# Kernel optimization log

Hardware: AMD Instinct MI355X
Metric: run time of the kernel (lower is better)

## Reference

```python
import jax, jax.numpy as jnp
import numpy as np

ALPHA = 0.2          # LeakyReLU negative slope
NEG_INF = -9e15      # mask value used by the torch module


def setup_inputs() -> dict:
    key = jax.random.key(0)
    k1, k2, k3, k4 = jax.random.split(key, 4)
    N, F_IN, F_OUT = 8192, 128, 128
    h = jax.random.normal(k1, (N, F_IN), dtype=jnp.float32)
    adj = jax.random.randint(k2, (N, N), 0, 2, dtype=jnp.int32)
    # xavier_uniform(gain=1.414) approximated with scaled normal init
    W = jax.random.normal(k3, (F_IN, F_OUT), dtype=jnp.float32) * (1.414 / np.sqrt(F_IN))
    a = jax.random.normal(k4, (2 * F_OUT, 1), dtype=jnp.float32) * (1.414 / np.sqrt(2 * F_OUT))
    return {"h": h, "adj": adj, "W": W, "a": a}


def reference(h, adj, W, a):
    # Wh: [N, F]
    Wh = h @ W
    F_out = W.shape[1]
    # e[i,j] = LeakyReLU( [Wh_i || Wh_j] . a ) = LeakyReLU( Wh_i.a1 + Wh_j.a2 )
    e_src = Wh @ a[:F_out, 0]   # [N]
    e_dst = Wh @ a[F_out:, 0]   # [N]
    e = jax.nn.leaky_relu(e_src[:, None] + e_dst[None, :], negative_slope=ALPHA)  # [N, N]
    attention = jax.nn.softmax(jnp.where(adj > 0, e, NEG_INF), axis=1)
    # dropout is identity in eval mode
    h_prime = attention @ Wh    # [N, F]
    return h_prime
```

## Files before the change

kernel.cpp:

```cpp
#include <hip/hip_runtime.h>
#include <hip/hip_bf16.h>


#define NN 8192
#define FF 128
#define SEG 4
#define JSEG (NN / SEG)
#define ITERS (JSEG / 64)

typedef __bf16 bf16x8 __attribute__((ext_vector_type(8)));
typedef float floatx4 __attribute__((ext_vector_type(4)));

__device__ __forceinline__ unsigned short f2b(float f) {
    unsigned int u = __float_as_uint(f);
    return (unsigned short)((u + 0x7FFFu + ((u >> 16) & 1u)) >> 16);
}

__global__ __launch_bounds__(128) void k0_uv(const float* __restrict__ W,
                                             const float* __restrict__ a,
                                             float* __restrict__ u,
                                             float* __restrict__ v) {
    int k = blockIdx.x, t = threadIdx.x;
    float wv = W[k * FF + t];
    float p1 = wv * a[t];
    float p2 = wv * a[FF + t];
    for (int off = 32; off; off >>= 1) {
        p1 += __shfl_down(p1, off);
        p2 += __shfl_down(p2, off);
    }
    __shared__ float r[4];
    if ((t & 63) == 0) { r[(t >> 6) * 2] = p1; r[(t >> 6) * 2 + 1] = p2; }
    __syncthreads();
    if (t == 0) { u[k] = r[0] + r[2]; v[k] = r[1] + r[3]; }
}

__global__ __launch_bounds__(256) void k1_wh(const float* __restrict__ h,
                                             const float* __restrict__ W,
                                             const float* __restrict__ u,
                                             const float* __restrict__ v,
                                             unsigned short* __restrict__ WhT,
                                             float* __restrict__ e_src,
                                             float* __restrict__ e_dst) {
    __shared__ float hL[32 * 132];
    __shared__ float wL[128 * 132];
    __shared__ float uL[128], vL[128];
    __shared__ unsigned short tL[128 * 40];

    int t = threadIdx.x;
    int i0 = blockIdx.x * 32;

    {
        int row = t >> 3, c = (t & 7) * 16;
        const float4* s = (const float4*)&h[(i0 + row) * FF + c];
        float4* d = (float4*)&hL[row * 132 + c];
        #pragma unroll
        for (int j = 0; j < 4; j++) d[j] = s[j];
    }
    {
        int row = t >> 1, c = (t & 1) * 64;
        const float4* s = (const float4*)&W[row * FF + c];
        float4* d = (float4*)&wL[row * 132 + c];
        #pragma unroll
        for (int j = 0; j < 16; j++) d[j] = s[j];
    }
    if (t < 128) { uL[t] = u[t]; vL[t] = v[t]; }
    __syncthreads();

    int r0 = (t & 7) * 4;
    int c0 = (t >> 3) * 4;
    float acc[4][4] = {};
    for (int k0 = 0; k0 < 128; k0 += 4) {
        float4 hr[4], wr[4];
        #pragma unroll
        for (int i = 0; i < 4; i++) hr[i] = *(const float4*)&hL[(r0 + i) * 132 + k0];
        #pragma unroll
        for (int i = 0; i < 4; i++) wr[i] = *(const float4*)&wL[(k0 + i) * 132 + c0];
        #pragma unroll
        for (int kj = 0; kj < 4; kj++) {
            #pragma unroll
            for (int ri = 0; ri < 4; ri++) {
                float hvv = ((const float*)&hr[ri])[kj];
                const float* wvv = (const float*)&wr[kj];
                #pragma unroll
                for (int cj = 0; cj < 4; cj++) acc[ri][cj] = fmaf(hvv, wvv[cj], acc[ri][cj]);
            }
        }
    }
    #pragma unroll
    for (int ri = 0; ri < 4; ri++)
        #pragma unroll
        for (int cj = 0; cj < 4; cj++)
            tL[(c0 + cj) * 40 + r0 + ri] = f2b(acc[ri][cj]);
    __syncthreads();

    if (t < 64) {
        int row = t & 31;
        const float* sv = (t < 32) ? uL : vL;
        float s = 0.f;
        for (int k = 0; k < 128; k += 4) {
            float4 h4 = *(const float4*)&hL[row * 132 + k];
            float4 s4 = *(const float4*)&sv[k];
            s = fmaf(h4.x, s4.x, s); s = fmaf(h4.y, s4.y, s);
            s = fmaf(h4.z, s4.z, s); s = fmaf(h4.w, s4.w, s);
        }
        (t < 32 ? e_src : e_dst)[i0 + row] = s;
    }
    {
        int f = t & 127, half = t >> 7;
        const uint4* s = (const uint4*)&tL[f * 40 + half * 16];
        uint4* d = (uint4*)&WhT[f * NN + i0 + half * 16];
        d[0] = s[0]; d[1] = s[1];
    }
}

__device__ __forceinline__ float mask_w(int a, float x) {
    float l = fmaxf(x, 0.2f * x);
    return a > 0 ? __expf(l) : 0.f;
}

__global__ __launch_bounds__(512, 4) void k2_gat(const int* __restrict__ adj,
                                                 const unsigned short* __restrict__ WhT,
                                                 const float* __restrict__ e_src,
                                                 const float* __restrict__ e_dst,
                                                 float* __restrict__ num,
                                                 float* __restrict__ den) {
    __shared__ unsigned short wt[2][32 * 64];
    __shared__ float esL[32];
    __shared__ float dpart[32 * 17];

    int t = threadIdx.x;
    int bx = blockIdx.x;
    int g = bx >> 2, seg = bx & 3;
    int i0 = g * 32;
    int jbase = seg * JSEG;

    if (t < 32) esL[t] = e_src[i0 + t];

    int ii = t & 31;
    int q  = t >> 5;
    int lane = t & 63, wave = t >> 6;
    int mrow = lane & 15, quad = lane >> 4;
    int n0 = wave * 16;

    const unsigned short* Bb = WhT + (size_t)(n0 + mrow) * NN + jbase + quad * 8;
    const int*   Ab = adj + (size_t)(i0 + ii) * NN + jbase + q * 4;
    const float* Eb = e_dst + jbase + q * 4;

    int waddr = ii * 64 + (((q >> 1) ^ (ii & 7)) << 3) + ((q & 1) << 2);
    int ra00 = mrow * 64 + ((quad ^ (mrow & 7)) << 3);
    int ra01 = mrow * 64 + (((4 + quad) ^ (mrow & 7)) << 3);
    int ra10 = (16 + mrow) * 64 + ((quad ^ (mrow & 7)) << 3);
    int ra11 = (16 + mrow) * 64 + (((4 + quad) ^ (mrow & 7)) << 3);

    floatx4 acc0 = {0.f, 0.f, 0.f, 0.f};
    floatx4 acc1 = {0.f, 0.f, 0.f, 0.f};
    float dsum = 0.f;
    __syncthreads();
    float es_i = esL[ii];

    int4   av = *(const int4*)Ab;
    float4 ed = *(const float4*)Eb;
    bf16x8 b0 = *(const bf16x8*)Bb;
    bf16x8 b1 = *(const bf16x8*)(Bb + 32);
    {
        float w0 = mask_w(av.x, es_i + ed.x);
        float w1 = mask_w(av.y, es_i + ed.y);
        float w2 = mask_w(av.z, es_i + ed.z);
        float w3 = mask_w(av.w, es_i + ed.w);
        dsum += (w0 + w1) + (w2 + w3);
        *(ushort4*)&wt[0][waddr] = make_ushort4(f2b(w0), f2b(w1), f2b(w2), f2b(w3));
    }
    __syncthreads();

    for (int k = 0; k < ITERS - 1; k++) {
        int joff = (k + 1) * 64;
        int4   av2 = *(const int4*)(Ab + joff);
        float4 ed2 = *(const float4*)(Eb + joff);
        bf16x8 nb0 = *(const bf16x8*)(Bb + joff);
        bf16x8 nb1 = *(const bf16x8*)(Bb + joff + 32);

        const unsigned short* buf = wt[k & 1];
        bf16x8 a00 = *(const bf16x8*)&buf[ra00];
        bf16x8 a10 = *(const bf16x8*)&buf[ra10];
        bf16x8 a01 = *(const bf16x8*)&buf[ra01];
        bf16x8 a11 = *(const bf16x8*)&buf[ra11];
        acc0 = __builtin_amdgcn_mfma_f32_16x16x32_bf16(a00, b0, acc0, 0, 0, 0);
        acc1 = __builtin_amdgcn_mfma_f32_16x16x32_bf16(a10, b0, acc1, 0, 0, 0);
        acc0 = __builtin_amdgcn_mfma_f32_16x16x32_bf16(a01, b1, acc0, 0, 0, 0);
        acc1 = __builtin_amdgcn_mfma_f32_16x16x32_bf16(a11, b1, acc1, 0, 0, 0);

        float w0 = mask_w(av2.x, es_i + ed2.x);
        float w1 = mask_w(av2.y, es_i + ed2.y);
        float w2 = mask_w(av2.z, es_i + ed2.z);
        float w3 = mask_w(av2.w, es_i + ed2.w);
        dsum += (w0 + w1) + (w2 + w3);
        *(ushort4*)&wt[(k + 1) & 1][waddr] = make_ushort4(f2b(w0), f2b(w1), f2b(w2), f2b(w3));
        b0 = nb0; b1 = nb1;
        __syncthreads();
    }
    {
        const unsigned short* buf = wt[(ITERS - 1) & 1];
        bf16x8 a00 = *(const bf16x8*)&buf[ra00];
        bf16x8 a10 = *(const bf16x8*)&buf[ra10];
        bf16x8 a01 = *(const bf16x8*)&buf[ra01];
        bf16x8 a11 = *(const bf16x8*)&buf[ra11];
        acc0 = __builtin_amdgcn_mfma_f32_16x16x32_bf16(a00, b0, acc0, 0, 0, 0);
        acc1 = __builtin_amdgcn_mfma_f32_16x16x32_bf16(a10, b0, acc1, 0, 0, 0);
        acc0 = __builtin_amdgcn_mfma_f32_16x16x32_bf16(a01, b1, acc0, 0, 0, 0);
        acc1 = __builtin_amdgcn_mfma_f32_16x16x32_bf16(a11, b1, acc1, 0, 0, 0);
    }

    dpart[ii * 17 + q] = dsum;
    __syncthreads();
    if (t < 32) {
        float s = 0.f;
        #pragma unroll
        for (int k = 0; k < 16; k++) s += dpart[t * 17 + k];
        atomicAdd(&den[i0 + t], s);
    }

    #pragma unroll
    for (int r = 0; r < 4; r++) {
        int row0 = quad * 4 + r;
        atomicAdd(&num[(size_t)(i0 + row0) * FF + n0 + mrow], acc0[r]);
        atomicAdd(&num[(size_t)(i0 + 16 + row0) * FF + n0 + mrow], acc1[r]);
    }
}

__global__ __launch_bounds__(256) void k3_scale(float* __restrict__ out,
                                                const float* __restrict__ den) {
    int idx = blockIdx.x * 256 + threadIdx.x;
    int i = idx >> 5;
    int c = (idx & 31) << 2;
    float r = 1.0f / den[i];
    float4* p = (float4*)&out[(size_t)i * FF + c];
    float4 v = *p;
    v.x *= r; v.y *= r; v.z *= r; v.w *= r;
    *p = v;
}

extern "C" void kernel_launch(void* const* d_in, const int* in_sizes, int n_in,
                              void* d_out, int out_size, void* d_ws, size_t ws_size,
                              hipStream_t stream) {
    const float* h   = (const float*)d_in[0];
    const int*   adj = (const int*)d_in[1];
    const float* W   = (const float*)d_in[2];
    const float* a   = (const float*)d_in[3];
    float* out = (float*)d_out;

    char* ws = (char*)d_ws;
    unsigned short* WhT = (unsigned short*)ws;
    float* u     = (float*)(ws + 2097152);
    float* v     = u + 128;
    float* e_src = v + 128;
    float* e_dst = e_src + NN;
    float* den   = e_dst + NN;

    hipMemsetAsync(out, 0, (size_t)NN * FF * sizeof(float), stream);
    hipMemsetAsync(den, 0, (size_t)NN * sizeof(float), stream);

    k0_uv<<<dim3(128), dim3(128), 0, stream>>>(W, a, u, v);
    k1_wh<<<dim3(256), dim3(256), 0, stream>>>(h, W, u, v, WhT, e_src, e_dst);
    k2_gat<<<dim3(256 * SEG), dim3(512), 0, stream>>>(adj, WhT, e_src, e_dst, out, den);
    k3_scale<<<dim3(NN * FF / 4 / 256), dim3(256), 0, stream>>>(out, den);
}
```

Before: 421.8 us.

## Replace atomic accumulation with per-segment partials and deepen adj prefetch

The attention kernel now writes per-segment numerator and denominator partials with nontemporal stores instead of float atomics. A merge kernel sums the four segments and normalises. This also removes the two memsets. The adjacency and e_dst loads are prefetched two iterations ahead, and the thread-to-row mapping is changed so each row's 64 columns come from 16 consecutive threads, giving more contiguous global reads. The cost is an extra 16 MB of partial writes and reads in the merge step.

```diff
diff --git a/kernel.cpp b/kernel.cpp
--- a/kernel.cpp
+++ b/kernel.cpp
@@ -122,8 +122,8 @@
                                                  const unsigned short* __restrict__ WhT,
                                                  const float* __restrict__ e_src,
                                                  const float* __restrict__ e_dst,
-                                                 float* __restrict__ num,
-                                                 float* __restrict__ den) {
+                                                 float* __restrict__ numpart,
+                                                 float* __restrict__ denpart) {
     __shared__ unsigned short wt[2][32 * 64];
     __shared__ float esL[32];
     __shared__ float dpart[32 * 17];
@@ -136,8 +136,8 @@
 
     if (t < 32) esL[t] = e_src[i0 + t];
 
-    int ii = t & 31;
-    int q  = t >> 5;
+    int q  = t & 15;
+    int ii = t >> 4;
     int lane = t & 63, wave = t >> 6;
     int mrow = lane & 15, quad = lane >> 4;
     int n0 = wave * 16;
@@ -155,29 +155,34 @@
     floatx4 acc0 = {0.f, 0.f, 0.f, 0.f};
     floatx4 acc1 = {0.f, 0.f, 0.f, 0.f};
     float dsum = 0.f;
-    __syncthreads();
-    float es_i = esL[ii];
-
-    int4   av = *(const int4*)Ab;
-    float4 ed = *(const float4*)Eb;
+
+    int4   av0 = *(const int4*)Ab;
+    float4 ed0 = *(const float4*)Eb;
+    int4   avB = *(const int4*)(Ab + 64);
+    float4 edB = *(const float4*)(Eb + 64);
     bf16x8 b0 = *(const bf16x8*)Bb;
     bf16x8 b1 = *(const bf16x8*)(Bb + 32);
-    {
-        float w0 = mask_w(av.x, es_i + ed.x);
-        float w1 = mask_w(av.y, es_i + ed.y);
-        float w2 = mask_w(av.z, es_i + ed.z);
-        float w3 = mask_w(av.w, es_i + ed.w);
+
+    __syncthreads();
+    float es_i = esL[ii];
+
+    {
+        float w0 = mask_w(av0.x, es_i + ed0.x);
+        float w1 = mask_w(av0.y, es_i + ed0.y);
+        float w2 = mask_w(av0.z, es_i + ed0.z);
+        float w3 = mask_w(av0.w, es_i + ed0.w);
         dsum += (w0 + w1) + (w2 + w3);
         *(ushort4*)&wt[0][waddr] = make_ushort4(f2b(w0), f2b(w1), f2b(w2), f2b(w3));
     }
     __syncthreads();
 
     for (int k = 0; k < ITERS - 1; k++) {
-        int joff = (k + 1) * 64;
-        int4   av2 = *(const int4*)(Ab + joff);
-        float4 ed2 = *(const float4*)(Eb + joff);
-        bf16x8 nb0 = *(const bf16x8*)(Bb + joff);
-        bf16x8 nb1 = *(const bf16x8*)(Bb + joff + 32);
+        int jp = ((k + 2 < ITERS) ? (k + 2) : (ITERS - 1)) * 64;
+        int4   avN = *(const int4*)(Ab + jp);
+        float4 edN = *(const float4*)(Eb + jp);
+        int jn = (k + 1) * 64;
+        bf16x8 nb0 = *(const bf16x8*)(Bb + jn);
+        bf16x8 nb1 = *(const bf16x8*)(Bb + jn + 32);
 
         const unsigned short* buf = wt[k & 1];
         bf16x8 a00 = *(const bf16x8*)&buf[ra00];
@@ -189,12 +194,13 @@
         acc0 = __builtin_amdgcn_mfma_f32_16x16x32_bf16(a01, b1, acc0, 0, 0, 0);
         acc1 = __builtin_amdgcn_mfma_f32_16x16x32_bf16(a11, b1, acc1, 0, 0, 0);
 
-        float w0 = mask_w(av2.x, es_i + ed2.x);
-        float w1 = mask_w(av2.y, es_i + ed2.y);
-        float w2 = mask_w(av2.z, es_i + ed2.z);
-        float w3 = mask_w(av2.w, es_i + ed2.w);
+        float w0 = mask_w(avB.x, es_i + edB.x);
+        float w1 = mask_w(avB.y, es_i + edB.y);
+        float w2 = mask_w(avB.z, es_i + edB.z);
+        float w3 = mask_w(avB.w, es_i + edB.w);
         dsum += (w0 + w1) + (w2 + w3);
         *(ushort4*)&wt[(k + 1) & 1][waddr] = make_ushort4(f2b(w0), f2b(w1), f2b(w2), f2b(w3));
+        avB = avN; edB = edN;
         b0 = nb0; b1 = nb1;
         __syncthreads();
     }
@@ -216,27 +222,38 @@
         float s = 0.f;
         #pragma unroll
         for (int k = 0; k < 16; k++) s += dpart[t * 17 + k];
-        atomicAdd(&den[i0 + t], s);
-    }
-
+        __builtin_nontemporal_store(s, &denpart[seg * NN + i0 + t]);
+    }
+
+    float* np = numpart + (size_t)seg * NN * FF;
     #pragma unroll
     for (int r = 0; r < 4; r++) {
         int row0 = quad * 4 + r;
-        atomicAdd(&num[(size_t)(i0 + row0) * FF + n0 + mrow], acc0[r]);
-        atomicAdd(&num[(size_t)(i0 + 16 + row0) * FF + n0 + mrow], acc1[r]);
-    }
-}
-
-__global__ __launch_bounds__(256) void k3_scale(float* __restrict__ out,
-                                                const float* __restrict__ den) {
+        __builtin_nontemporal_store(acc0[r], &np[(size_t)(i0 + row0) * FF + n0 + mrow]);
+        __builtin_nontemporal_store(acc1[r], &np[(size_t)(i0 + 16 + row0) * FF + n0 + mrow]);
+    }
+}
+
+__global__ __launch_bounds__(256) void k3_merge(const float* __restrict__ np,
+                                               const float* __restrict__ dp,
+                                               float* __restrict__ out) {
     int idx = blockIdx.x * 256 + threadIdx.x;
     int i = idx >> 5;
     int c = (idx & 31) << 2;
-    float r = 1.0f / den[i];
-    float4* p = (float4*)&out[(size_t)i * FF + c];
-    float4 v = *p;
-    v.x *= r; v.y *= r; v.z *= r; v.w *= r;
-    *p = v;
+    float d = dp[i] + dp[NN + i] + dp[2 * NN + i] + dp[3 * NN + i];
+    float r = 1.0f / d;
+    size_t o = (size_t)i * FF + c;
+    const size_t S = (size_t)NN * FF;
+    float4 a0 = *(const float4*)&np[o];
+    float4 a1 = *(const float4*)&np[o + S];
+    float4 a2 = *(const float4*)&np[o + 2 * S];
+    float4 a3 = *(const float4*)&np[o + 3 * S];
+    float4 v;
+    v.x = ((a0.x + a1.x) + (a2.x + a3.x)) * r;
+    v.y = ((a0.y + a1.y) + (a2.y + a3.y)) * r;
+    v.z = ((a0.z + a1.z) + (a2.z + a3.z)) * r;
+    v.w = ((a0.w + a1.w) + (a2.w + a3.w)) * r;
+    *(float4*)&out[o] = v;
 }
 
 extern "C" void kernel_launch(void* const* d_in, const int* in_sizes, int n_in,
@@ -254,13 +271,11 @@
     float* v     = u + 128;
     float* e_src = v + 128;
     float* e_dst = e_src + NN;
-    float* den   = e_dst + NN;
-
-    hipMemsetAsync(out, 0, (size_t)NN * FF * sizeof(float), stream);
-    hipMemsetAsync(den, 0, (size_t)NN * sizeof(float), stream);
+    float* denpart = e_dst + NN;
+    float* numpart = (float*)(ws + (4u << 20));
 
     k0_uv<<<dim3(128), dim3(128), 0, stream>>>(W, a, u, v);
     k1_wh<<<dim3(256), dim3(256), 0, stream>>>(h, W, u, v, WhT, e_src, e_dst);
-    k2_gat<<<dim3(256 * SEG), dim3(512), 0, stream>>>(adj, WhT, e_src, e_dst, out, den);
-    k3_scale<<<dim3(NN * FF / 4 / 256), dim3(256), 0, stream>>>(out, den);
-}
+    k2_gat<<<dim3(256 * SEG), dim3(512), 0, stream>>>(adj, WhT, e_src, e_dst, numpart, denpart);
+    k3_merge<<<dim3(NN * FF / 4 / 256), dim3(256), 0, stream>>>(numpart, denpart, out);
+}
```

Result: faster. 404.3 us (-4.1%).
